# Optimization experiments

Hardware: AMD Instinct MI355X
Metric: run time of the kernel (lower is better)

## Reference

```python
import jax, jax.numpy as jnp
import numpy as np

T = 2048          # tokens (batch*seq flattened, vLLM style)
HID = 2048        # hidden size
NH = 16           # attention heads
QLR, KVLR = 1536, 512            # q / kv lora ranks
DN, DR, DV = 128, 64, 128        # qk_nope, qk_rope, v head dims
QKD = DN + DR                    # 192
INH, IHD = 16, 128               # indexer heads / head dim
ITOPK = 512                      # indexer top-k keys per query
E, EK, MI = 8, 4, 512            # routed experts, experts per token, expert intermediate
SH_MI = 1024                     # shared expert intermediate
EPS = 1e-6
ROUTED_SCALE = 1.0


def rms_norm(x, w, eps=EPS):
    v = jnp.mean(jnp.square(x), axis=-1, keepdims=True)
    return x * jax.lax.rsqrt(v + eps) * w


def layer_norm(x, w, b, eps=EPS):
    m = jnp.mean(x, axis=-1, keepdims=True)
    v = jnp.var(x, axis=-1, keepdims=True)
    return (x - m) * jax.lax.rsqrt(v + eps) * w + b


def rope(x, pos):
    """Neox-style rotary over the full last dim. x: [T, D] or [T, H, D]."""
    D = x.shape[-1]
    half = D // 2
    inv = 1.0 / (10000.0 ** (jnp.arange(half, dtype=jnp.float32) / half))
    f = pos.astype(jnp.float32)[:, None] * inv                  # [T, half]
    cos, sin = jnp.cos(f), jnp.sin(f)
    if x.ndim == 3:
        cos, sin = cos[:, None, :], sin[:, None, :]
    x1, x2 = x[..., :half], x[..., half:]
    return jnp.concatenate([x1 * cos - x2 * sin, x1 * sin + x2 * cos], axis=-1)


def setup_inputs() -> dict:
    key = jax.random.key(0)
    ks = jax.random.split(key, 16)

    def w(k, shape, fan_in):
        return (jax.random.normal(k, shape, jnp.float32) / np.sqrt(fan_in)).astype(jnp.float32)

    return {
        "positions": jnp.arange(T, dtype=jnp.int32),
        "hidden_states": jax.random.normal(ks[0], (T, HID), jnp.float32),
        "ln1_w": jnp.ones((HID,), jnp.float32),
        "ln2_w": jnp.ones((HID,), jnp.float32),
        "w_qkv_a": w(ks[1], (HID, QLR + KVLR + DR), HID),
        "q_a_ln_w": jnp.ones((QLR,), jnp.float32),
        "kv_a_ln_w": jnp.ones((KVLR,), jnp.float32),
        "w_q_b": w(ks[2], (QLR, NH * QKD), QLR),
        "w_kv_b": w(ks[3], (KVLR, NH * (DN + DV)), KVLR),
        "w_o": w(ks[4], (NH * DV, HID), NH * DV),
        "w_idx_k": w(ks[5], (HID, IHD), HID),
        "idx_k_ln_w": jnp.ones((IHD,), jnp.float32),
        "idx_k_ln_b": jnp.zeros((IHD,), jnp.float32),
        "w_idx_qb": w(ks[6], (QLR, INH * IHD), QLR),
        "w_idx_w": w(ks[7], (HID, INH), HID),
        "w_gate": w(ks[8], (HID, E), HID),
        "w_moe_gu": w(ks[9], (E, HID, 2 * MI), HID),
        "w_moe_d": w(ks[10], (E, MI, HID), MI),
        "w_sh_gu": w(ks[11], (HID, 2 * SH_MI), HID),
        "w_sh_d": w(ks[12], (SH_MI, HID), SH_MI),
    }


def reference(positions, hidden_states, ln1_w, ln2_w, w_qkv_a, q_a_ln_w, kv_a_ln_w,
              w_q_b, w_kv_b, w_o, w_idx_k, idx_k_ln_w, idx_k_ln_b, w_idx_qb,
              w_idx_w, w_gate, w_moe_gu, w_moe_d, w_sh_gu, w_sh_d):
    # residual is None on entry -> residual = hidden_states; h = rms_norm(h)
    residual = hidden_states
    h = rms_norm(hidden_states, ln1_w)

    # fused_qkv_a_proj -> split into q latent, kv latent, rope key
    qkv = h @ w_qkv_a
    q_c = rms_norm(qkv[:, :QLR], q_a_ln_w)                      # q_a_layernorm
    kv_c = rms_norm(qkv[:, QLR:QLR + KVLR], kv_a_ln_w)          # kv_a_layernorm
    k_pe = rope(qkv[:, QLR + KVLR:], positions)                 # [T, DR]

    # indexer key path: wk -> LayerNorm(w,b) -> rope on trailing DR dims
    idx_k = layer_norm(h @ w_idx_k, idx_k_ln_w, idx_k_ln_b)     # [T, IHD]
    idx_k = jnp.concatenate([idx_k[:, :IHD - DR], rope(idx_k[:, IHD - DR:], positions)], axis=-1)

    # query path: q_b projection, rope on the rope slice per head
    q = (q_c @ w_q_b).reshape(T, NH, QKD)
    q = jnp.concatenate([q[..., :DN], rope(q[..., DN:], positions)], axis=-1)

    # indexer query + per-query head weights (scale folds quant scale role in float ref)
    idx_q = (q_c @ w_idx_qb).reshape(T, INH, IHD)
    idx_q = jnp.concatenate([idx_q[..., :IHD - DR], rope(idx_q[..., IHD - DR:], positions)], axis=-1)
    idx_w = (h @ w_idx_w) * (IHD ** -0.5) * (INH ** -0.5)       # [T, INH]

    # lightning indexer: score[t,s] = sum_h w[t,h] * relu(q[t,h] . k[s])
    ilogits = jnp.einsum('thd,sd->ths', idx_q, idx_k)           # [T, INH, T]
    iscores = jnp.einsum('ths,th->ts', jax.nn.relu(ilogits), idx_w)
    causal = positions[:, None] >= positions[None, :]
    neg = jnp.finfo(iscores.dtype).min
    iscores = jnp.where(causal, iscores, neg)
    _, top_idx = jax.lax.top_k(iscores, ITOPK)                  # [T, ITOPK]
    sel = jnp.zeros((T, T), bool).at[jnp.arange(T)[:, None], top_idx].set(True)
    amask = sel & causal                                        # sparse attention mask

    # MLA attention (unabsorbed form): expand kv latent to per-head k_nope, v
    kv = (kv_c @ w_kv_b).reshape(T, NH, DN + DV)
    k_nope, v = kv[..., :DN], kv[..., DN:]
    alogits = (jnp.einsum('thd,shd->hts', q[..., :DN], k_nope)
               + jnp.einsum('thd,sd->hts', q[..., DN:], k_pe)) * (QKD ** -0.5)
    alogits = jnp.where(amask[None], alogits, neg)
    probs = jax.nn.softmax(alogits, axis=-1)
    attn = jnp.einsum('hts,shd->thd', probs, v).reshape(T, NH * DV)

    # o_proj + fused_add_rms_norm
    residual = residual + attn @ w_o
    h = rms_norm(residual, ln2_w)

    # MoE: softmax gate -> top-k, renormalize, dense combine + shared expert
    g = jax.nn.softmax(h @ w_gate, axis=-1)                     # [T, E]
    tv, ti = jax.lax.top_k(g, EK)
    tw = tv / jnp.sum(tv, axis=-1, keepdims=True)
    dense_w = jnp.zeros((T, E), h.dtype).at[jnp.arange(T)[:, None], ti].set(tw)
    gu = jnp.einsum('th,ehm->tem', h, w_moe_gu)                 # [T, E, 2*MI]
    act = jax.nn.silu(gu[..., :MI]) * gu[..., MI:]
    down = jnp.einsum('tem,emh->teh', act, w_moe_d)             # [T, E, HID]
    routed = jnp.einsum('teh,te->th', down, dense_w) * ROUTED_SCALE
    sgu = h @ w_sh_gu
    shared = (jax.nn.silu(sgu[:, :SH_MI]) * sgu[:, SH_MI:]) @ w_sh_d
    out = routed + shared
    return out, residual
```

## Files before the change

### kernel.cpp

```cpp
#include <hip/hip_runtime.h>
#include <cstdint>
#include <cstddef>

#define T_TOK 2048
#define HIDN  2048
#define NHEAD 16
#define QLRr  1536
#define KVLRr 512
#define DNn   128
#define DRr   64
#define DVv   128
#define QKDd  192
#define INHh  16
#define IHDd  128
#define ITOPKk 512
#define NEXP  8
#define MIi   512
#define SHMI  1024
#define EPSF  1e-6f
#define NEGINF (-3.402823466e38f)

typedef __attribute__((ext_vector_type(8))) short short8;
typedef __attribute__((ext_vector_type(4))) float float4v;

__device__ __forceinline__ float warp_sum(float v){
#pragma unroll
  for (int off=32; off>0; off>>=1) v += __shfl_down(v, off, 64);
  return v;
}
__device__ __forceinline__ float warp_max(float v){
#pragma unroll
  for (int off=32; off>0; off>>=1) v = fmaxf(v, __shfl_down(v, off, 64));
  return v;
}
__device__ __forceinline__ unsigned mapf(float f){
  unsigned b = __float_as_uint(f);
  if ((b<<1)==0u) b = 0u;
  return (b & 0x80000000u) ? ~b : (b | 0x80000000u);
}
__device__ __forceinline__ ushort f2bf(float f){
  unsigned u = __float_as_uint(f);
  unsigned r = (u + 0x7fffu + ((u>>16)&1u)) >> 16;
  return (ushort)r;
}
__device__ __forceinline__ float bf2f(ushort u){
  return __uint_as_float(((unsigned)u) << 16);
}

__global__ void rope_table_kernel(const int* __restrict__ pos,
                                  float* __restrict__ ct, float* __restrict__ st){
  int t = blockIdx.x, j = threadIdx.x;
  float inv = powf(10000.0f, -(float)j * (1.0f/32.0f));
  float f = (float)pos[t] * inv;
  ct[t*32+j] = cosf(f);
  st[t*32+j] = sinf(f);
}

__global__ __launch_bounds__(256) void rmsnorm_kernel(
    const float* __restrict__ x, int xstride, int xoff,
    const float* __restrict__ w, float* __restrict__ out, int ostride, int D){
  int t = blockIdx.x, tid = threadIdx.x;
  const float* xp = x + (size_t)t*xstride + xoff;
  const float4* x4 = (const float4*)xp;
  int D4 = D >> 2;
  float ss = 0.f;
  for (int i = tid; i < D4; i += 256){ float4 v = x4[i]; ss += v.x*v.x+v.y*v.y+v.z*v.z+v.w*v.w; }
  __shared__ float red[4];
  float s = warp_sum(ss);
  int lane = tid & 63, wid = tid >> 6;
  if (lane==0) red[wid] = s;
  __syncthreads();
  if (tid==0) red[0] = red[0]+red[1]+red[2]+red[3];
  __syncthreads();
  float sc = rsqrtf(red[0]/(float)D + EPSF);
  const float4* w4 = (const float4*)w;
  float4* o4 = (float4*)(out + (size_t)t*ostride);
  for (int i = tid; i < D4; i += 256){
    float4 v = x4[i], ww = w4[i];
    float4 r; r.x=v.x*sc*ww.x; r.y=v.y*sc*ww.y; r.z=v.z*sc*ww.z; r.w=v.w*sc*ww.w;
    o4[i] = r;
  }
}

__global__ void rope_kpe_kernel(const float* __restrict__ pe,
                                const float* __restrict__ ct, const float* __restrict__ st,
                                float* __restrict__ kpe){
  int t = blockIdx.x, j = threadIdx.x;
  const float* x = pe + (size_t)t*64;
  float x1 = x[j], x2 = x[32+j];
  float c = ct[t*32+j], sn = st[t*32+j];
  kpe[t*64+j]    = x1*c - x2*sn;
  kpe[t*64+32+j] = x1*sn + x2*c;
}

__global__ __launch_bounds__(128) void ln_rope_idxk_kernel(
    float* __restrict__ xk, const float* __restrict__ w, const float* __restrict__ b,
    const float* __restrict__ ct, const float* __restrict__ st){
  int t = blockIdx.x, tid = threadIdx.x;
  float v = xk[(size_t)t*IHDd + tid];
  float s1 = warp_sum(v), s2 = warp_sum(v*v);
  __shared__ float r1[2], r2[2];
  int lane = tid & 63, wid = tid >> 6;
  if (lane==0){ r1[wid]=s1; r2[wid]=s2; }
  __syncthreads();
  float mean = (r1[0]+r1[1]) * (1.f/128.f);
  float var  = (r2[0]+r2[1]) * (1.f/128.f) - mean*mean;
  float y = (v-mean)*rsqrtf(var+EPSF)*w[tid]+b[tid];
  __shared__ float ly[128];
  ly[tid] = y; __syncthreads();
  float o;
  if (tid < 64) o = y;
  else if (tid < 96){ int j = tid-64; o = ly[64+j]*ct[t*32+j] - ly[96+j]*st[t*32+j]; }
  else              { int j = tid-96; o = ly[64+j]*st[t*32+j] + ly[96+j]*ct[t*32+j]; }
  xk[(size_t)t*IHDd + tid] = o;
}

__global__ __launch_bounds__(256) void rope_q_kernel(float* __restrict__ q,
                                  const float* __restrict__ ct, const float* __restrict__ st){
  int t = blockIdx.x, tid = threadIdx.x;
  __shared__ float c[32], s[32];
  if (tid < 32){ c[tid]=ct[t*32+tid]; s[tid]=st[t*32+tid]; }
  __syncthreads();
  for (int idx = tid; idx < NHEAD*32; idx += 256){
    int hh = idx >> 5, j = idx & 31;
    float* base = q + (size_t)t*(NHEAD*QKDd) + hh*QKDd;
    float x1 = base[DNn+j], x2 = base[DNn+32+j];
    base[DNn+j]    = x1*c[j] - x2*s[j];
    base[DNn+32+j] = x1*s[j] + x2*c[j];
  }
}

__global__ __launch_bounds__(256) void rope_idxq_kernel(float* __restrict__ q,
                                  const float* __restrict__ ct, const float* __restrict__ st){
  int t = blockIdx.x, tid = threadIdx.x;
  __shared__ float c[32], s[32];
  if (tid < 32){ c[tid]=ct[t*32+tid]; s[tid]=st[t*32+tid]; }
  __syncthreads();
  for (int idx = tid; idx < INHh*32; idx += 256){
    int hh = idx >> 5, j = idx & 31;
    float* base = q + (size_t)t*(INHh*IHDd) + hh*IHDd;
    float x1 = base[64+j], x2 = base[96+j];
    base[64+j] = x1*c[j] - x2*s[j];
    base[96+j] = x1*s[j] + x2*c[j];
  }
}

__global__ __launch_bounds__(256) void gemm_f32(
    const float* __restrict__ A, int lda,
    const float* __restrict__ B, int ldb,
    float* __restrict__ C, int ldc,
    const float* __restrict__ addsrc, int ldadd,
    int M, int N, int K, float alpha){
  __shared__ float As[16][68];
  __shared__ float Bs[16][68];
  int tid = threadIdx.x;
  int tx = tid & 15, ty = tid >> 4;
  int m0 = blockIdx.y*64, n0 = blockIdx.x*64;
  float acc[4][4] = {};
  for (int k0 = 0; k0 < K; k0 += 16){
#pragma unroll
    for (int i = 0; i < 4; i++){
      int lin = tid + i*256; int r = lin >> 4, c = lin & 15;
      int m = m0 + r;
      As[c][r] = (m < M) ? A[(size_t)m*lda + k0 + c] : 0.f;
    }
#pragma unroll
    for (int i = 0; i < 4; i++){
      int lin = tid + i*256; int kk = lin >> 6, c = lin & 63;
      int n = n0 + c;
      Bs[kk][c] = (n < N) ? B[(size_t)(k0+kk)*ldb + n] : 0.f;
    }
    __syncthreads();
#pragma unroll
    for (int kk = 0; kk < 16; kk++){
      float4 av = *(const float4*)&As[kk][ty*4];
      float4 bv = *(const float4*)&Bs[kk][tx*4];
      float a[4] = {av.x, av.y, av.z, av.w};
      float b[4] = {bv.x, bv.y, bv.z, bv.w};
#pragma unroll
      for (int i = 0; i < 4; i++)
#pragma unroll
        for (int j = 0; j < 4; j++) acc[i][j] += a[i]*b[j];
    }
    __syncthreads();
  }
#pragma unroll
  for (int i = 0; i < 4; i++){
    int m = m0 + ty*4 + i;
    if (m >= M) continue;
#pragma unroll
    for (int j = 0; j < 4; j++){
      int n = n0 + tx*4 + j;
      if (n >= N) continue;
      float v = acc[i][j]*alpha;
      if (addsrc) v += addsrc[(size_t)m*ldadd + n];
      C[(size_t)m*ldc + n] = v;
    }
  }
}

__global__ __launch_bounds__(256) void conv_bf16(const float* __restrict__ in,
                                                 ushort* __restrict__ out, int n4){
  int i = blockIdx.x*256 + threadIdx.x;
  if (i < n4){
    float4 v = ((const float4*)in)[i];
    ushort4 o; o.x=f2bf(v.x); o.y=f2bf(v.y); o.z=f2bf(v.z); o.w=f2bf(v.w);
    ((ushort4*)out)[i] = o;
  }
}

__global__ __launch_bounds__(256) void split_bf16(const float* __restrict__ in,
                                                  ushort* __restrict__ hi,
                                                  ushort* __restrict__ lo, int n4){
  int i = blockIdx.x*256 + threadIdx.x;
  if (i >= n4) return;
  float4 v = ((const float4*)in)[i];
  ushort4 h, l;
  h.x = f2bf(v.x); l.x = f2bf(v.x - bf2f(h.x));
  h.y = f2bf(v.y); l.y = f2bf(v.y - bf2f(h.y));
  h.z = f2bf(v.z); l.z = f2bf(v.z - bf2f(h.z));
  h.w = f2bf(v.w); l.w = f2bf(v.w - bf2f(h.w));
  ((ushort4*)hi)[i] = h;
  ((ushort4*)lo)[i] = l;
}

__global__ __launch_bounds__(256) void transconv(const float* __restrict__ src0,
                                                 ushort* __restrict__ dst0, int K, int N){
  int e = blockIdx.z;
  const float* src = src0 + (size_t)e*K*N;
  ushort* dst = dst0 + (size_t)e*N*K;
  int k0 = blockIdx.y*32, n0 = blockIdx.x*32;
  __shared__ float tile[32][33];
  int c = threadIdx.x & 31, r = threadIdx.x >> 5;
  for (int rr = r; rr < 32; rr += 8) tile[rr][c] = src[(size_t)(k0+rr)*N + n0 + c];
  __syncthreads();
  for (int rr = r; rr < 32; rr += 8) dst[(size_t)(n0+rr)*K + k0 + c] = f2bf(tile[c][rr]);
}

__global__ __launch_bounds__(256) void transconv_split(const float* __restrict__ src,
                                                       ushort* __restrict__ dhi,
                                                       ushort* __restrict__ dlo, int K, int N){
  int k0 = blockIdx.y*32, n0 = blockIdx.x*32;
  __shared__ float tile[32][33];
  int c = threadIdx.x & 31, r = threadIdx.x >> 5;
  for (int rr = r; rr < 32; rr += 8) tile[rr][c] = src[(size_t)(k0+rr)*N + n0 + c];
  __syncthreads();
  for (int rr = r; rr < 32; rr += 8){
    float x = tile[c][rr];
    ushort h = f2bf(x);
    ushort l = f2bf(x - bf2f(h));
    size_t o = (size_t)(n0+rr)*K + k0 + c;
    dhi[o] = h; dlo[o] = l;
  }
}

__global__ __launch_bounds__(256) void gemm_b3(
    const ushort* __restrict__ Ah, const ushort* __restrict__ Al,
    const ushort* __restrict__ Bh, const ushort* __restrict__ Bl,
    float* __restrict__ C, const float* __restrict__ addsrc, int N, int K){
  __shared__ __align__(16) ushort Ahs[5120], Als[5120];
  __shared__ __align__(16) ushort Bhs[5120], Bls[5120];
  int tid = threadIdx.x, lane = tid & 63, w = tid >> 6;
  int m0 = blockIdx.y*128, n0 = blockIdx.x*128;
  int wr = w >> 1, wc = w & 1;
  int r15 = lane & 15, g = lane >> 4;
  int srow = tid >> 1, sh = (tid & 1) << 4;
  size_t arow = (size_t)(m0 + srow)*K + sh;
  size_t brow = (size_t)(n0 + srow)*K + sh;
  int soff = srow*40 + sh;
  int aoff[4], boff[4];
#pragma unroll
  for (int m = 0; m < 4; m++){
    aoff[m] = (wr*64 + m*16 + r15)*40 + g*8;
    boff[m] = (wc*64 + m*16 + r15)*40 + g*8;
  }
  float4v acc[4][4];
#pragma unroll
  for (int i=0;i<4;i++)
#pragma unroll
    for (int j=0;j<4;j++) acc[i][j] = (float4v){0.f,0.f,0.f,0.f};
  int nk = K >> 5;
  for (int kt = 0; kt < nk; kt++){
    int k0 = kt << 5;
    short8 ah0 = *(const short8*)(Ah + arow + k0);
    short8 ah1 = *(const short8*)(Ah + arow + k0 + 8);
    short8 al0 = *(const short8*)(Al + arow + k0);
    short8 al1 = *(const short8*)(Al + arow + k0 + 8);
    short8 bh0 = *(const short8*)(Bh + brow + k0);
    short8 bh1 = *(const short8*)(Bh + brow + k0 + 8);
    short8 bl0 = *(const short8*)(Bl + brow + k0);
    short8 bl1 = *(const short8*)(Bl + brow + k0 + 8);
    __syncthreads();
    *(short8*)&Ahs[soff] = ah0; *(short8*)&Ahs[soff+8] = ah1;
    *(short8*)&Als[soff] = al0; *(short8*)&Als[soff+8] = al1;
    *(short8*)&Bhs[soff] = bh0; *(short8*)&Bhs[soff+8] = bh1;
    *(short8*)&Bls[soff] = bl0; *(short8*)&Bls[soff+8] = bl1;
    __syncthreads();
    short8 avh[4], avl[4], bvh[4], bvl[4];
#pragma unroll
    for (int m = 0; m < 4; m++){
      avh[m] = *(const short8*)&Ahs[aoff[m]];
      avl[m] = *(const short8*)&Als[aoff[m]];
    }
#pragma unroll
    for (int n = 0; n < 4; n++){
      bvh[n] = *(const short8*)&Bhs[boff[n]];
      bvl[n] = *(const short8*)&Bls[boff[n]];
    }
#pragma unroll
    for (int m = 0; m < 4; m++)
#pragma unroll
      for (int n = 0; n < 4; n++){
        acc[m][n] = __builtin_amdgcn_mfma_f32_16x16x32_bf16(avh[m], bvh[n], acc[m][n], 0, 0, 0);
        acc[m][n] = __builtin_amdgcn_mfma_f32_16x16x32_bf16(avl[m], bvh[n], acc[m][n], 0, 0, 0);
        acc[m][n] = __builtin_amdgcn_mfma_f32_16x16x32_bf16(avh[m], bvl[n], acc[m][n], 0, 0, 0);
      }
  }
#pragma unroll
  for (int m = 0; m < 4; m++){
    int row0 = m0 + wr*64 + m*16 + g*4;
#pragma unroll
    for (int n = 0; n < 4; n++){
      int col = n0 + wc*64 + n*16 + r15;
#pragma unroll
      for (int r = 0; r < 4; r++){
        float v = acc[m][n][r];
        size_t o = (size_t)(row0 + r)*N + col;
        if (addsrc) v += addsrc[o];
        C[o] = v;
      }
    }
  }
}

template<int OUTBF>
__global__ __launch_bounds__(256) void gemm_bf16s(
    const ushort* __restrict__ A, const ushort* __restrict__ Bt,
    float* __restrict__ Cf, ushort* __restrict__ Cb,
    const float* __restrict__ addsrc, int N, int K){
  __shared__ __align__(16) ushort As[5120];
  __shared__ __align__(16) ushort Bs[5120];
  int tid = threadIdx.x, lane = tid & 63, w = tid >> 6;
  int m0 = blockIdx.y*128, n0 = blockIdx.x*128;
  int wr = w >> 1, wc = w & 1;
  int r15 = lane & 15, g = lane >> 4;
  int srow = tid >> 1, sh = (tid & 1) << 4;
  const ushort* Ag = A + (size_t)(m0 + srow)*K + sh;
  const ushort* Bg = Bt + (size_t)(n0 + srow)*K + sh;
  ushort* Asw = &As[srow*40 + sh];
  ushort* Bsw = &Bs[srow*40 + sh];
  int aoff[4], boff[4];
#pragma unroll
  for (int m = 0; m < 4; m++){
    aoff[m] = (wr*64 + m*16 + r15)*40 + g*8;
    boff[m] = (wc*64 + m*16 + r15)*40 + g*8;
  }
  float4v acc[4][4];
#pragma unroll
  for (int i=0;i<4;i++)
#pragma unroll
    for (int j=0;j<4;j++) acc[i][j] = (float4v){0.f,0.f,0.f,0.f};
  int nk = K >> 5;
  for (int kt = 0; kt < nk; kt++){
    int k0 = kt << 5;
    short8 a0 = *(const short8*)(Ag + k0);
    short8 a1 = *(const short8*)(Ag + k0 + 8);
    short8 b0 = *(const short8*)(Bg + k0);
    short8 b1 = *(const short8*)(Bg + k0 + 8);
    __syncthreads();
    *(short8*)Asw = a0; *(short8*)(Asw + 8) = a1;
    *(short8*)Bsw = b0; *(short8*)(Bsw + 8) = b1;
    __syncthreads();
    short8 av[4], bv[4];
#pragma unroll
    for (int m = 0; m < 4; m++) av[m] = *(const short8*)&As[aoff[m]];
#pragma unroll
    for (int n = 0; n < 4; n++) bv[n] = *(const short8*)&Bs[boff[n]];
#pragma unroll
    for (int m = 0; m < 4; m++)
#pragma unroll
      for (int n = 0; n < 4; n++)
        acc[m][n] = __builtin_amdgcn_mfma_f32_16x16x32_bf16(av[m], bv[n], acc[m][n], 0, 0, 0);
  }
#pragma unroll
  for (int m = 0; m < 4; m++){
    int row0 = m0 + wr*64 + m*16 + g*4;
#pragma unroll
    for (int n = 0; n < 4; n++){
      int col = n0 + wc*64 + n*16 + r15;
#pragma unroll
      for (int r = 0; r < 4; r++){
        float v = acc[m][n][r];
        size_t o = (size_t)(row0 + r)*N + col;
        if (addsrc) v += addsrc[o];
        if (OUTBF) Cb[o] = f2bf(v);
        else       Cf[o] = v;
      }
    }
  }
}

__global__ __launch_bounds__(256) void moe_gemm1s(
    const ushort* __restrict__ h2bf, const ushort* __restrict__ wgut,
    const int* __restrict__ ecnt, const int* __restrict__ elist,
    float* __restrict__ gu){
  int e = blockIdx.z;
  int count = ecnt[e];
  int r0 = blockIdx.y*128;
  if (r0 >= count) return;
  __shared__ int rows[128];
  __shared__ __align__(16) ushort As[5120];
  __shared__ __align__(16) ushort Bs[5120];
  int tid = threadIdx.x, lane = tid & 63, w = tid >> 6;
  int n0 = blockIdx.x*128;
  if (tid < 128) rows[tid] = (r0 + tid < count) ? elist[e*2048 + r0 + tid] : -1;
  __syncthreads();
  int wr = w >> 1, wc = w & 1;
  int r15 = lane & 15, g = lane >> 4;
  int srow = tid >> 1, sh = (tid & 1) << 4;
  int ent0 = rows[srow];
  int tok = (ent0 >= 0) ? (ent0 >> 2) : 0;
  const ushort* Ag = h2bf + (size_t)tok*2048 + sh;
  const ushort* Bg = wgut + ((size_t)e*1024 + n0 + srow)*2048 + sh;
  ushort* Asw = &As[srow*40 + sh];
  ushort* Bsw = &Bs[srow*40 + sh];
  int aoff[4], boff[4];
#pragma unroll
  for (int m = 0; m < 4; m++){
    aoff[m] = (wr*64 + m*16 + r15)*40 + g*8;
    boff[m] = (wc*64 + m*16 + r15)*40 + g*8;
  }
  float4v acc[4][4];
#pragma unroll
  for (int i=0;i<4;i++)
#pragma unroll
    for (int j=0;j<4;j++) acc[i][j] = (float4v){0.f,0.f,0.f,0.f};
  for (int kt = 0; kt < 64; kt++){
    int k0 = kt << 5;
    short8 a0 = *(const short8*)(Ag + k0);
    short8 a1 = *(const short8*)(Ag + k0 + 8);
    short8 b0 = *(const short8*)(Bg + k0);
    short8 b1 = *(const short8*)(Bg + k0 + 8);
    __syncthreads();
    *(short8*)Asw = a0; *(short8*)(Asw + 8) = a1;
    *(short8*)Bsw = b0; *(short8*)(Bsw + 8) = b1;
    __syncthreads();
    short8 av[4], bv[4];
#pragma unroll
    for (int m = 0; m < 4; m++) av[m] = *(const short8*)&As[aoff[m]];
#pragma unroll
    for (int n = 0; n < 4; n++) bv[n] = *(const short8*)&Bs[boff[n]];
#pragma unroll
    for (int m = 0; m < 4; m++)
#pragma unroll
      for (int n = 0; n < 4; n++)
        acc[m][n] = __builtin_amdgcn_mfma_f32_16x16x32_bf16(av[m], bv[n], acc[m][n], 0, 0, 0);
  }
#pragma unroll
  for (int m = 0; m < 4; m++){
#pragma unroll
    for (int r = 0; r < 4; r++){
      int ent = rows[wr*64 + m*16 + g*4 + r];
      if (ent < 0) continue;
#pragma unroll
      for (int n = 0; n < 4; n++){
        int col = n0 + wc*64 + n*16 + r15;
        gu[(size_t)ent*1024 + col] = acc[m][n][r];
      }
    }
  }
}

__global__ __launch_bounds__(256) void moe_gemm2s(
    const ushort* __restrict__ act, const ushort* __restrict__ wdt,
    const int* __restrict__ ecnt, const int* __restrict__ elist,
    const float* __restrict__ tw, float* __restrict__ down){
  int e = blockIdx.z;
  int count = ecnt[e];
  int r0 = blockIdx.y*128;
  if (r0 >= count) return;
  __shared__ int rows[128];
  __shared__ __align__(16) ushort As[5120];
  __shared__ __align__(16) ushort Bs[5120];
  int tid = threadIdx.x, lane = tid & 63, w = tid >> 6;
  int n0 = blockIdx.x*128;
  if (tid < 128) rows[tid] = (r0 + tid < count) ? elist[e*2048 + r0 + tid] : -1;
  __syncthreads();
  int wr = w >> 1, wc = w & 1;
  int r15 = lane & 15, g = lane >> 4;
  int srow = tid >> 1, sh = (tid & 1) << 4;
  int ent0 = rows[srow];
  int src = (ent0 >= 0) ? ent0 : 0;
  const ushort* Ag = act + (size_t)src*512 + sh;
  const ushort* Bg = wdt + ((size_t)e*2048 + n0 + srow)*512 + sh;
  ushort* Asw = &As[srow*40 + sh];
  ushort* Bsw = &Bs[srow*40 + sh];
  int aoff[4], boff[4];
#pragma unroll
  for (int m = 0; m < 4; m++){
    aoff[m] = (wr*64 + m*16 + r15)*40 + g*8;
    boff[m] = (wc*64 + m*16 + r15)*40 + g*8;
  }
  float4v acc[4][4];
#pragma unroll
  for (int i=0;i<4;i++)
#pragma unroll
    for (int j=0;j<4;j++) acc[i][j] = (float4v){0.f,0.f,0.f,0.f};
  for (int kt = 0; kt < 16; kt++){
    int k0 = kt << 5;
    short8 a0 = *(const short8*)(Ag + k0);
    short8 a1 = *(const short8*)(Ag + k0 + 8);
    short8 b0 = *(const short8*)(Bg + k0);
    short8 b1 = *(const short8*)(Bg + k0 + 8);
    __syncthreads();
    *(short8*)Asw = a0; *(short8*)(Asw + 8) = a1;
    *(short8*)Bsw = b0; *(short8*)(Bsw + 8) = b1;
    __syncthreads();
    short8 av[4], bv[4];
#pragma unroll
    for (int m = 0; m < 4; m++) av[m] = *(const short8*)&As[aoff[m]];
#pragma unroll
    for (int n = 0; n < 4; n++) bv[n] = *(const short8*)&Bs[boff[n]];
#pragma unroll
    for (int m = 0; m < 4; m++)
#pragma unroll
      for (int n = 0; n < 4; n++)
        acc[m][n] = __builtin_amdgcn_mfma_f32_16x16x32_bf16(av[m], bv[n], acc[m][n], 0, 0, 0);
  }
#pragma unroll
  for (int m = 0; m < 4; m++){
#pragma unroll
    for (int r = 0; r < 4; r++){
      int ent = rows[wr*64 + m*16 + g*4 + r];
      if (ent < 0) continue;
      float wgt = tw[ent];
#pragma unroll
      for (int n = 0; n < 4; n++){
        int col = n0 + wc*64 + n*16 + r15;
        down[(size_t)ent*2048 + col] = acc[m][n][r]*wgt;
      }
    }
  }
}

__global__ __launch_bounds__(256) void iscores_kernel(
    const float* __restrict__ idx_q, const float* __restrict__ idx_k,
    const float* __restrict__ idx_w, float* __restrict__ sc){
  int sb = blockIdx.x, tb = blockIdx.y;
  if (sb > tb) return;
  int t0 = tb*64, s0 = sb*64;
  __shared__ float As[32][68];
  __shared__ float Bs[32][68];
  __shared__ float Ws[64][17];
  int tid = threadIdx.x, tx = tid & 15, ty = tid >> 4;
  for (int i = tid; i < 1024; i += 256){ int r = i >> 4, hh = i & 15; Ws[r][hh] = idx_w[(size_t)(t0+r)*16 + hh]; }
  float sco[4][4] = {};
  for (int h = 0; h < 16; h++){
    float acc[4][4] = {};
    for (int k0 = 0; k0 < 128; k0 += 32){
#pragma unroll
      for (int i = 0; i < 8; i++){
        int lin = tid + i*256; int r = lin >> 5, c = lin & 31;
        As[c][r] = idx_q[(size_t)(t0+r)*2048 + h*128 + k0 + c];
      }
#pragma unroll
      for (int i = 0; i < 8; i++){
        int lin = tid + i*256; int r = lin >> 5, c = lin & 31;
        Bs[c][r] = idx_k[(size_t)(s0+r)*128 + k0 + c];
      }
      __syncthreads();
#pragma unroll
      for (int kk = 0; kk < 32; kk++){
        float4 av = *(const float4*)&As[kk][ty*4];
        float4 bv = *(const float4*)&Bs[kk][tx*4];
        float a[4] = {av.x, av.y, av.z, av.w};
        float b[4] = {bv.x, bv.y, bv.z, bv.w};
#pragma unroll
        for (int i = 0; i < 4; i++)
#pragma unroll
          for (int j = 0; j < 4; j++) acc[i][j] += a[i]*b[j];
      }
      __syncthreads();
    }
#pragma unroll
    for (int i = 0; i < 4; i++){
      float wv = Ws[ty*4+i][h];
#pragma unroll
      for (int j = 0; j < 4; j++) sco[i][j] += wv * fmaxf(acc[i][j], 0.f);
    }
  }
#pragma unroll
  for (int i = 0; i < 4; i++){
    int tg = t0 + ty*4 + i;
#pragma unroll
    for (int j = 0; j < 4; j++){
      int sg = s0 + tx*4 + j;
      sc[(size_t)tg*2048 + sg] = (sg <= tg) ? sco[i][j] : NEGINF;
    }
  }
}

__global__ __launch_bounds__(256) void topk_kernel(
    const float* __restrict__ scores, int* __restrict__ list, int* __restrict__ cnt){
  int t = blockIdx.x, tid = threadIdx.x;
  if (t < ITOPKk){
    for (int i = tid; i <= t; i += 256) list[(size_t)t*ITOPKk + i] = i;
    if (tid==0) cnt[t] = t+1;
    return;
  }
  int n = t+1;
  const float* row = scores + (size_t)t*2048;
  __shared__ unsigned hist[256];
  __shared__ unsigned sh_prefix, sh_krem;
  __shared__ int scan[256];
  __shared__ int sh_base_sel, sh_base_eq;
  if (tid==0){ sh_prefix = 0u; sh_krem = ITOPKk; }
  __syncthreads();
  for (int level = 3; level >= 0; level--){
    int shift = level*8;
    hist[tid] = 0u; __syncthreads();
    unsigned pfx = sh_prefix;
    for (int s = tid; s < n; s += 256){
      unsigned u = mapf(row[s]);
      bool ok = (level==3) || ((u >> (shift+8)) == pfx);
      if (ok) atomicAdd(&hist[(u >> shift) & 255u], 1u);
    }
    __syncthreads();
    if (tid==0){
      unsigned krem = sh_krem, c = 0u; int bsel = 0;
      for (int b = 255; b >= 0; b--){
        if (c + hist[b] >= krem){ bsel = b; break; }
        c += hist[b];
      }
      sh_prefix = (pfx << 8) | (unsigned)bsel;
      sh_krem = krem - c;
    }
    __syncthreads();
  }
  unsigned uth = sh_prefix; int R = (int)sh_krem;
  if (tid==0){ sh_base_sel = 0; sh_base_eq = 0; }
  __syncthreads();
  for (int c0 = 0; c0 < n; c0 += 256){
    int s = c0 + tid;
    unsigned u = (s < n) ? mapf(row[s]) : 0u;
    int gt = (s < n) && (u > uth);
    int eq = (s < n) && (u == uth);
    scan[tid] = (eq << 16) | gt; __syncthreads();
    for (int off = 1; off < 256; off <<= 1){
      int v = (tid >= off) ? scan[tid-off] : 0; __syncthreads();
      scan[tid] += v; __syncthreads();
    }
    int incl = scan[tid];
    int gt_incl = incl & 0xffff, eq_incl = incl >> 16;
    int gt_excl = gt_incl - gt, eq_excl = eq_incl - eq;
    int tot = scan[255]; int gt_tot = tot & 0xffff, eq_tot = tot >> 16;
    int base_sel = sh_base_sel, base_eq = sh_base_eq;
    int rtake = R - base_eq; if (rtake < 0) rtake = 0;
    bool selected = gt || (eq && eq_excl < rtake);
    int pos = base_sel + gt_excl + min(eq_excl, rtake);
    if (selected) list[(size_t)t*ITOPKk + pos] = s;
    __syncthreads();
    if (tid==0){
      sh_base_sel = base_sel + gt_tot + min(eq_tot, rtake);
      sh_base_eq  = base_eq + eq_tot;
    }
    __syncthreads();
  }
  if (tid==0) cnt[t] = ITOPKk;
}

#define HG 2
__global__ __launch_bounds__(256) void attn_kernel(
    const float* __restrict__ q, const float* __restrict__ kv,
    const float* __restrict__ kpe,
    const int* __restrict__ list, const int* __restrict__ cnt,
    float* __restrict__ attn){
  int b = blockIdx.x;
  int g8 = b & 7, t = b >> 3;
  int h0 = g8*HG;
  int tid = threadIdx.x, lane = tid & 63, w = tid >> 6;
  __shared__ int   sl[ITOPKk];
  __shared__ float qs[HG][200];
  __shared__ float lg[HG][ITOPKk];
  __shared__ float redm[4], reds[4];
  __shared__ float4 outp4[8][32];
  int n = cnt[t];
  for (int i = tid; i < n; i += 256) sl[i] = list[(size_t)t*ITOPKk + i];
  for (int i = tid; i < HG*192; i += 256){
    int hh = i/192, d = i - hh*192;
    qs[hh][d] = q[(size_t)t*(NHEAD*QKDd) + (h0+hh)*QKDd + d];
  }
  __syncthreads();
  const float scale = 0.07216878364870323f;
  int half = lane >> 5, l5 = lane & 31;
  for (int i = w; i < n; i += 4){
    int s = sl[i];
    float4 k4 = *(const float4*)(kv + (size_t)s*4096 + (h0+half)*256 + l5*4);
    float2 pe2 = *(const float2*)(kpe + (size_t)s*64 + l5*2);
    float4 qv = *(const float4*)&qs[half][l5*4];
    float pk = k4.x*qv.x + k4.y*qv.y + k4.z*qv.z + k4.w*qv.w;
    pk += pe2.x*qs[half][128 + l5*2] + pe2.y*qs[half][128 + l5*2 + 1];
    pk += __shfl_down(pk, 16, 32);
    pk += __shfl_down(pk, 8, 32);
    pk += __shfl_down(pk, 4, 32);
    pk += __shfl_down(pk, 2, 32);
    pk += __shfl_down(pk, 1, 32);
    if (l5 == 0) lg[half][i] = pk*scale;
  }
  __syncthreads();
  int slice = tid & 31, sg = tid >> 5;
  for (int hh = 0; hh < HG; hh++){
    int h = h0 + hh;
    float mx = NEGINF;
    for (int i = tid; i < n; i += 256) mx = fmaxf(mx, lg[hh][i]);
    mx = warp_max(mx);
    if (lane==0) redm[w] = mx;
    __syncthreads();
    mx = fmaxf(fmaxf(redm[0],redm[1]), fmaxf(redm[2],redm[3]));
    float sum = 0.f;
    for (int i = tid; i < n; i += 256){ float p = expf(lg[hh][i]-mx); lg[hh][i] = p; sum += p; }
    sum = warp_sum(sum);
    if (lane==0) reds[w] = sum;
    __syncthreads();
    float inv = 1.f/(reds[0]+reds[1]+reds[2]+reds[3]);
    float4 acc = {0,0,0,0};
    for (int i = sg; i < n; i += 8){
      float p = lg[hh][i];
      float4 v4 = *((const float4*)(kv + (size_t)sl[i]*4096 + h*256 + 128) + slice);
      acc.x += p*v4.x; acc.y += p*v4.y; acc.z += p*v4.z; acc.w += p*v4.w;
    }
    outp4[sg][slice] = acc;
    __syncthreads();
    if (tid < 32){
      float4 r = outp4[0][tid];
#pragma unroll
      for (int gg = 1; gg < 8; gg++){
        float4 o = outp4[gg][tid];
        r.x += o.x; r.y += o.y; r.z += o.z; r.w += o.w;
      }
      r.x *= inv; r.y *= inv; r.z *= inv; r.w *= inv;
      *(float4*)&attn[(size_t)t*2048 + h*128 + tid*4] = r;
    }
    __syncthreads();
  }
}

__global__ void gate_kernel(const float* __restrict__ glog, float* __restrict__ tw,
                            int* __restrict__ ecnt, int* __restrict__ elist){
  int t = blockIdx.x*256 + threadIdx.x;
  if (t >= T_TOK) return;
  float g[8]; float mx = NEGINF;
  for (int i = 0; i < 8; i++){ g[i] = glog[t*8+i]; mx = fmaxf(mx, g[i]); }
  float s = 0.f;
  for (int i = 0; i < 8; i++){ g[i] = expf(g[i]-mx); s += g[i]; }
  for (int i = 0; i < 8; i++) g[i] /= s;
  bool used[8] = {};
  float tv[4]; int si[4];
  for (int k = 0; k < 4; k++){
    float best = -1.f; int bi = 0;
    for (int i = 0; i < 8; i++) if (!used[i] && g[i] > best){ best = g[i]; bi = i; }
    used[bi] = true; tv[k] = best; si[k] = bi;
  }
  float s4 = tv[0]+tv[1]+tv[2]+tv[3];
  for (int k = 0; k < 4; k++){
    tw[t*4+k] = tv[k]/s4;
    int pos = atomicAdd(&ecnt[si[k]], 1);
    elist[si[k]*2048 + pos] = t*4+k;
  }
}

__global__ __launch_bounds__(256) void silu_moe(const float* __restrict__ gu,
                                                ushort* __restrict__ act){
  int i = blockIdx.x*256 + threadIdx.x;
  if (i >= 8192*128) return;
  int row = i >> 7, jc = i & 127;
  float4 g4 = ((const float4*)(gu + (size_t)row*1024))[jc];
  float4 u4 = ((const float4*)(gu + (size_t)row*1024 + 512))[jc];
  ushort4 o;
  o.x = f2bf(g4.x/(1.f+expf(-g4.x))*u4.x);
  o.y = f2bf(g4.y/(1.f+expf(-g4.y))*u4.y);
  o.z = f2bf(g4.z/(1.f+expf(-g4.z))*u4.z);
  o.w = f2bf(g4.w/(1.f+expf(-g4.w))*u4.w);
  ((ushort4*)(act + (size_t)row*512))[jc] = o;
}

__global__ __launch_bounds__(256) void moe_combine(const float* __restrict__ down,
                                                   float* __restrict__ outf){
  int t = blockIdx.x;
  size_t base = (size_t)t*4*2048;
  for (int d = threadIdx.x; d < 2048; d += 256){
    float s = down[base+d] + down[base+2048+d] + down[base+4096+d] + down[base+6144+d];
    outf[(size_t)t*2048 + d] += s;
  }
}

__global__ __launch_bounds__(256) void silu_sh(const float* __restrict__ sgu,
                                               ushort* __restrict__ shact){
  int i = blockIdx.x*256 + threadIdx.x;
  if (i >= 2048*256) return;
  int row = i >> 8, jc = i & 255;
  float4 g4 = ((const float4*)(sgu + (size_t)row*2048))[jc];
  float4 u4 = ((const float4*)(sgu + (size_t)row*2048 + 1024))[jc];
  ushort4 o;
  o.x = f2bf(g4.x/(1.f+expf(-g4.x))*u4.x);
  o.y = f2bf(g4.y/(1.f+expf(-g4.y))*u4.y);
  o.z = f2bf(g4.z/(1.f+expf(-g4.z))*u4.z);
  o.w = f2bf(g4.w/(1.f+expf(-g4.w))*u4.w);
  ((ushort4*)(shact + (size_t)row*1024))[jc] = o;
}

extern "C" void kernel_launch(void* const* d_in, const int* in_sizes, int n_in,
                              void* d_out, int out_size, void* d_ws, size_t ws_size,
                              hipStream_t stream){
  const int*   positions  = (const int*)  d_in[0];
  const float* hidden     = (const float*)d_in[1];
  const float* ln1_w      = (const float*)d_in[2];
  const float* ln2_w      = (const float*)d_in[3];
  const float* w_qkv_a    = (const float*)d_in[4];
  const float* q_a_ln_w   = (const float*)d_in[5];
  const float* kv_a_ln_w  = (const float*)d_in[6];
  const float* w_q_b      = (const float*)d_in[7];
  const float* w_kv_b     = (const float*)d_in[8];
  const float* w_o        = (const float*)d_in[9];
  const float* w_idx_k    = (const float*)d_in[10];
  const float* idx_k_ln_w = (const float*)d_in[11];
  const float* idx_k_ln_b = (const float*)d_in[12];
  const float* w_idx_qb   = (const float*)d_in[13];
  const float* w_idx_w    = (const float*)d_in[14];
  const float* w_gate     = (const float*)d_in[15];
  const float* w_moe_gu   = (const float*)d_in[16];
  const float* w_moe_d    = (const float*)d_in[17];
  const float* w_sh_gu    = (const float*)d_in[18];
  const float* w_sh_d     = (const float*)d_in[19];

  float* out_final = (float*)d_out;
  float* residual  = (float*)d_out + (size_t)T_TOK*HIDN;

  float* ws = (float*)d_ws;
  float* arena   = ws;
  float* qkv_main= arena;
  float* qkv_pe  = arena + 4194304;
  float* iscores = arena;
  float* qbuf    = arena + 4325376;
  float* idx_q   = arena + 10616832;
  float* q_c     = arena + 14811136;
  float* kv_c    = arena + 17956864;
  float* sgu     = arena;
  float* gu_buf  = arena;
  float* down_buf= arena;
  ushort* act_bf = (ushort*)(arena + 16777216);
  ushort* h_hi  = (ushort*)(arena + 4325376);
  ushort* h_lo  = h_hi + 4194304;
  ushort* wqa_hi= (ushort*)(arena + 8519680);
  ushort* wqa_lo= wqa_hi + 4325376;
  ushort* wik_hi= (ushort*)(arena + 12845056);
  ushort* wik_lo= wik_hi + 262144;
  ushort* qc2_hi= (ushort*)arena;
  ushort* qc2_lo= qc2_hi + 3145728;
  ushort* wiq_hi= (ushort*)(arena + 4325376);
  ushort* wiq_lo= wiq_hi + 3145728;
  ushort* s1 = (ushort*)arena;
  ushort* s2 = (ushort*)(arena + 10616832);
  size_t off = 19005440;
  float* h      = ws + off; off += 4194304;
  float* kv     = ws + off; off += 8388608;
  float* attnbuf= ws + off; off += 4194304;
  float* k_pe   = ws + off; off += 131072;
  float* idx_k  = ws + off; off += 262144;
  float* idx_w  = ws + off; off += 32768;
  float* glog   = ws + off; off += 16384;
  float* tw     = ws + off; off += 8192;
  float* ctab   = ws + off; off += 65536;
  float* stab   = ws + off; off += 65536;
  int* list     = (int*)(ws + off);
  int* cnt      = list + 1048576;
  int* ecnt     = cnt + 2048;
  int* elist    = ecnt + 8;
  off += 1067016;
  ushort* h2_bf   = (ushort*)(ws + off);
  off += 2097152;
  ushort* shact_bf= (ushort*)(ws + off);
  off += 1048576;
  ushort* wshgu_t = (ushort*)(ws + off);
  off += 2097152;
  ushort* wshd_t  = (ushort*)(ws + off);
  off += 1048576;
  ushort* wmgu_t = (ushort*)kv;
  ushort* wmd_t  = (ushort*)attnbuf;
  size_t total_bytes = off * sizeof(float);
  if (ws_size < total_bytes) return;

  ushort* qc_hi  = s1;
  ushort* qc_lo  = s1 + 3145728;
  ushort* wqbt_hi= s2;
  ushort* wqbt_lo= s2 + 4718592;
  ushort* kvc_hi = s1;
  ushort* kvc_lo = s1 + 1048576;
  ushort* wkvt_hi= s1 + 2097152;
  ushort* wkvt_lo= s1 + 4194304;
  ushort* at_hi  = s2;
  ushort* at_lo  = s2 + 4194304;
  ushort* wot_hi = s1;
  ushort* wot_lo = s1 + 4194304;

  transconv<<<dim3(64,64,1), 256, 0, stream>>>(w_sh_gu, wshgu_t, 2048, 2048);
  transconv<<<dim3(64,32,1), 256, 0, stream>>>(w_sh_d,  wshd_t,  1024, 2048);

  rope_table_kernel<<<T_TOK, 32, 0, stream>>>(positions, ctab, stab);
  rmsnorm_kernel<<<T_TOK, 256, 0, stream>>>(hidden, HIDN, 0, ln1_w, h, HIDN, HIDN);
  split_bf16<<<4096, 256, 0, stream>>>(h, h_hi, h_lo, 1048576);
  transconv_split<<<dim3(66,64), 256, 0, stream>>>(w_qkv_a, wqa_hi, wqa_lo, 2048, 2112);
  gemm_b3<<<dim3(16,16), 256, 0, stream>>>(h_hi, h_lo, wqa_hi, wqa_lo, qkv_main, nullptr, 2048, 2048);
  gemm_f32<<<dim3(1,32), 256, 0, stream>>>(h, HIDN, w_qkv_a + 2048, 2112, qkv_pe, 64, nullptr, 0, T_TOK, 64, HIDN, 1.f);
  rmsnorm_kernel<<<T_TOK, 256, 0, stream>>>(qkv_main, 2048, 0,    q_a_ln_w,  q_c,  QLRr,  QLRr);
  rmsnorm_kernel<<<T_TOK, 256, 0, stream>>>(qkv_main, 2048, QLRr, kv_a_ln_w, kv_c, KVLRr, KVLRr);
  rope_kpe_kernel<<<T_TOK, 32, 0, stream>>>(qkv_pe, ctab, stab, k_pe);
  transconv_split<<<dim3(4,64), 256, 0, stream>>>(w_idx_k, wik_hi, wik_lo, 2048, 128);
  gemm_b3<<<dim3(1,16), 256, 0, stream>>>(h_hi, h_lo, wik_hi, wik_lo, idx_k, nullptr, 128, 2048);
  ln_rope_idxk_kernel<<<T_TOK, 128, 0, stream>>>(idx_k, idx_k_ln_w, idx_k_ln_b, ctab, stab);
  split_bf16<<<3072, 256, 0, stream>>>(q_c, qc2_hi, qc2_lo, 786432);
  transconv_split<<<dim3(64,48), 256, 0, stream>>>(w_idx_qb, wiq_hi, wiq_lo, 1536, 2048);
  gemm_b3<<<dim3(16,16), 256, 0, stream>>>(qc2_hi, qc2_lo, wiq_hi, wiq_lo, idx_q, nullptr, 2048, 1536);
  rope_idxq_kernel<<<T_TOK, 256, 0, stream>>>(idx_q, ctab, stab);
  gemm_f32<<<dim3(1,32), 256, 0, stream>>>(h, HIDN, w_idx_w, INHh, idx_w, INHh, nullptr, 0, T_TOK, INHh, HIDN, 0.02209708691207961f);
  iscores_kernel<<<dim3(32,32), 256, 0, stream>>>(idx_q, idx_k, idx_w, iscores);
  topk_kernel<<<T_TOK, 256, 0, stream>>>(iscores, list, cnt);
  split_bf16<<<3072, 256, 0, stream>>>(q_c, qc_hi, qc_lo, 786432);
  transconv_split<<<dim3(96,48), 256, 0, stream>>>(w_q_b, wqbt_hi, wqbt_lo, 1536, 3072);
  gemm_b3<<<dim3(24,16), 256, 0, stream>>>(qc_hi, qc_lo, wqbt_hi, wqbt_lo, qbuf, nullptr, 3072, 1536);
  rope_q_kernel<<<T_TOK, 256, 0, stream>>>(qbuf, ctab, stab);
  split_bf16<<<1024, 256, 0, stream>>>(kv_c, kvc_hi, kvc_lo, 262144);
  transconv_split<<<dim3(128,16), 256, 0, stream>>>(w_kv_b, wkvt_hi, wkvt_lo, 512, 4096);
  gemm_b3<<<dim3(32,16), 256, 0, stream>>>(kvc_hi, kvc_lo, wkvt_hi, wkvt_lo, kv, nullptr, 4096, 512);
  attn_kernel<<<T_TOK*(NHEAD/HG), 256, 0, stream>>>(qbuf, kv, k_pe, list, cnt, attnbuf);
  split_bf16<<<4096, 256, 0, stream>>>(attnbuf, at_hi, at_lo, 1048576);
  transconv_split<<<dim3(64,64), 256, 0, stream>>>(w_o, wot_hi, wot_lo, 2048, 2048);
  gemm_b3<<<dim3(16,16), 256, 0, stream>>>(at_hi, at_lo, wot_hi, wot_lo, residual, hidden, 2048, 2048);
  transconv<<<dim3(32,64,8), 256, 0, stream>>>(w_moe_gu, wmgu_t, 2048, 1024);
  transconv<<<dim3(64,16,8), 256, 0, stream>>>(w_moe_d,  wmd_t,  512,  2048);
  rmsnorm_kernel<<<T_TOK, 256, 0, stream>>>(residual, HIDN, 0, ln2_w, h, HIDN, HIDN);
  gemm_f32<<<dim3(1,32), 256, 0, stream>>>(h, HIDN, w_gate, NEXP, glog, NEXP, nullptr, 0, T_TOK, NEXP, HIDN, 1.f);
  hipMemsetAsync(ecnt, 0, NEXP*sizeof(int), stream);
  gate_kernel<<<8, 256, 0, stream>>>(glog, tw, ecnt, elist);
  conv_bf16<<<4096, 256, 0, stream>>>(h, h2_bf, 1048576);
  gemm_bf16s<0><<<dim3(16,16), 256, 0, stream>>>(h2_bf, wshgu_t, sgu, nullptr, nullptr, 2048, 2048);
  silu_sh<<<2048, 256, 0, stream>>>(sgu, shact_bf);
  gemm_bf16s<0><<<dim3(16,16), 256, 0, stream>>>(shact_bf, wshd_t, out_final, nullptr, nullptr, 2048, 1024);
  moe_gemm1s<<<dim3(8, 16, NEXP), 256, 0, stream>>>(h2_bf, wmgu_t, ecnt, elist, gu_buf);
  silu_moe<<<4096, 256, 0, stream>>>(gu_buf, act_bf);
  moe_gemm2s<<<dim3(16, 16, NEXP), 256, 0, stream>>>(act_bf, wmd_t, ecnt, elist, tw, down_buf);
  moe_combine<<<T_TOK, 256, 0, stream>>>(down_buf, out_final);
  (void)in_sizes; (void)n_in; (void)out_size;
}
```

Measured before the change: 2.760 ms.

## Compute indexer scores with split-bf16 MFMA and reuse the q_c bf16 split

Replaces the fp32 SIMT indexer-score kernel with a 128x128-tile MFMA kernel. It uses a three-product hi/lo bf16 split to keep near-fp32 accuracy, and applies the per-head ReLU and weighted sum in the accumulator epilogue. Adds split_bf16 passes for idx_q and idx_k. The q_c split is now done once and shared by the indexer and q_b GEMMs. Workspace aliases are reshuffled (qc and kvc moved into the kv and attnbuf regions, kv_c split moved earlier) so the new buffers don't clobber live data. The explicit causal -inf fill on diagonal tiles is dropped, which relies on topk reading only the first t+1 entries.

```diff
diff --git a/kernel.cpp b/kernel.cpp
--- a/kernel.cpp
+++ b/kernel.cpp
@@ -333,6 +333,107 @@
   }
 }
 
+__global__ __launch_bounds__(256) void iscores_b3(
+    const ushort* __restrict__ iqh, const ushort* __restrict__ iql,
+    const ushort* __restrict__ ikh, const ushort* __restrict__ ikl,
+    const float* __restrict__ idx_w,
+    float* __restrict__ sc){
+  int sb = blockIdx.x, tb = blockIdx.y;
+  if (sb > tb) return;
+  int t0 = tb*128, s0 = sb*128;
+  __shared__ __align__(16) ushort Ahs[5120], Als[5120];
+  __shared__ __align__(16) ushort Bhs[5120], Bls[5120];
+  __shared__ float wlds[128][17];
+  int tid = threadIdx.x, lane = tid & 63, w = tid >> 6;
+  int wr = w >> 1, wc = w & 1;
+  int r15 = lane & 15, g = lane >> 4;
+  int srow = tid >> 1, sh = (tid & 1) << 4;
+  for (int i = tid; i < 2048; i += 256){
+    int r = i >> 4, hh = i & 15;
+    wlds[r][hh] = idx_w[(size_t)(t0+r)*16 + hh];
+  }
+  int soff = srow*40 + sh;
+  int aoff[4], boff[4];
+#pragma unroll
+  for (int m = 0; m < 4; m++){
+    aoff[m] = (wr*64 + m*16 + r15)*40 + g*8;
+    boff[m] = (wc*64 + m*16 + r15)*40 + g*8;
+  }
+  float4v sco[4][4];
+#pragma unroll
+  for (int i=0;i<4;i++)
+#pragma unroll
+    for (int j=0;j<4;j++) sco[i][j] = (float4v){0.f,0.f,0.f,0.f};
+  for (int h = 0; h < 16; h++){
+    float4v acc[4][4];
+#pragma unroll
+    for (int i=0;i<4;i++)
+#pragma unroll
+      for (int j=0;j<4;j++) acc[i][j] = (float4v){0.f,0.f,0.f,0.f};
+    size_t arow = ((size_t)(t0 + srow)*16 + h)*128 + sh;
+    size_t brow = (size_t)(s0 + srow)*128 + sh;
+#pragma unroll
+    for (int kt = 0; kt < 4; kt++){
+      int k0 = kt << 5;
+      short8 ah0 = *(const short8*)(iqh + arow + k0);
+      short8 ah1 = *(const short8*)(iqh + arow + k0 + 8);
+      short8 al0 = *(const short8*)(iql + arow + k0);
+      short8 al1 = *(const short8*)(iql + arow + k0 + 8);
+      short8 bh0 = *(const short8*)(ikh + brow + k0);
+      short8 bh1 = *(const short8*)(ikh + brow + k0 + 8);
+      short8 bl0 = *(const short8*)(ikl + brow + k0);
+      short8 bl1 = *(const short8*)(ikl + brow + k0 + 8);
+      __syncthreads();
+      *(short8*)&Ahs[soff] = ah0; *(short8*)&Ahs[soff+8] = ah1;
+      *(short8*)&Als[soff] = al0; *(short8*)&Als[soff+8] = al1;
+      *(short8*)&Bhs[soff] = bh0; *(short8*)&Bhs[soff+8] = bh1;
+      *(short8*)&Bls[soff] = bl0; *(short8*)&Bls[soff+8] = bl1;
+      __syncthreads();
+      short8 avh[4], avl[4], bvh[4], bvl[4];
+#pragma unroll
+      for (int m = 0; m < 4; m++){
+        avh[m] = *(const short8*)&Ahs[aoff[m]];
+        avl[m] = *(const short8*)&Als[aoff[m]];
+      }
+#pragma unroll
+      for (int n = 0; n < 4; n++){
+        bvh[n] = *(const short8*)&Bhs[boff[n]];
+        bvl[n] = *(const short8*)&Bls[boff[n]];
+      }
+#pragma unroll
+      for (int m = 0; m < 4; m++)
+#pragma unroll
+        for (int n = 0; n < 4; n++){
+          acc[m][n] = __builtin_amdgcn_mfma_f32_16x16x32_bf16(avh[m], bvh[n], acc[m][n], 0, 0, 0);
+          acc[m][n] = __builtin_amdgcn_mfma_f32_16x16x32_bf16(avl[m], bvh[n], acc[m][n], 0, 0, 0);
+          acc[m][n] = __builtin_amdgcn_mfma_f32_16x16x32_bf16(avh[m], bvl[n], acc[m][n], 0, 0, 0);
+        }
+    }
+#pragma unroll
+    for (int m = 0; m < 4; m++){
+      int rbase = wr*64 + m*16 + g*4;
+#pragma unroll
+      for (int r = 0; r < 4; r++){
+        float wv = wlds[rbase + r][h];
+#pragma unroll
+        for (int n = 0; n < 4; n++)
+          sco[m][n][r] += wv * fmaxf(acc[m][n][r], 0.f);
+      }
+    }
+  }
+#pragma unroll
+  for (int m = 0; m < 4; m++){
+    int row0 = t0 + wr*64 + m*16 + g*4;
+#pragma unroll
+    for (int n = 0; n < 4; n++){
+      int col = s0 + wc*64 + n*16 + r15;
+#pragma unroll
+      for (int r = 0; r < 4; r++)
+        sc[(size_t)(row0 + r)*2048 + col] = sco[m][n][r];
+    }
+  }
+}
+
 template<int OUTBF>
 __global__ __launch_bounds__(256) void gemm_bf16s(
     const ushort* __restrict__ A, const ushort* __restrict__ Bt,
@@ -539,63 +640,6 @@
         int col = n0 + wc*64 + n*16 + r15;
         down[(size_t)ent*2048 + col] = acc[m][n][r]*wgt;
       }
-    }
-  }
-}
-
-__global__ __launch_bounds__(256) void iscores_kernel(
-    const float* __restrict__ idx_q, const float* __restrict__ idx_k,
-    const float* __restrict__ idx_w, float* __restrict__ sc){
-  int sb = blockIdx.x, tb = blockIdx.y;
-  if (sb > tb) return;
-  int t0 = tb*64, s0 = sb*64;
-  __shared__ float As[32][68];
-  __shared__ float Bs[32][68];
-  __shared__ float Ws[64][17];
-  int tid = threadIdx.x, tx = tid & 15, ty = tid >> 4;
-  for (int i = tid; i < 1024; i += 256){ int r = i >> 4, hh = i & 15; Ws[r][hh] = idx_w[(size_t)(t0+r)*16 + hh]; }
-  float sco[4][4] = {};
-  for (int h = 0; h < 16; h++){
-    float acc[4][4] = {};
-    for (int k0 = 0; k0 < 128; k0 += 32){
-#pragma unroll
-      for (int i = 0; i < 8; i++){
-        int lin = tid + i*256; int r = lin >> 5, c = lin & 31;
-        As[c][r] = idx_q[(size_t)(t0+r)*2048 + h*128 + k0 + c];
-      }
-#pragma unroll
-      for (int i = 0; i < 8; i++){
-        int lin = tid + i*256; int r = lin >> 5, c = lin & 31;
-        Bs[c][r] = idx_k[(size_t)(s0+r)*128 + k0 + c];
-      }
-      __syncthreads();
-#pragma unroll
-      for (int kk = 0; kk < 32; kk++){
-        float4 av = *(const float4*)&As[kk][ty*4];
-        float4 bv = *(const float4*)&Bs[kk][tx*4];
-        float a[4] = {av.x, av.y, av.z, av.w};
-        float b[4] = {bv.x, bv.y, bv.z, bv.w};
-#pragma unroll
-        for (int i = 0; i < 4; i++)
-#pragma unroll
-          for (int j = 0; j < 4; j++) acc[i][j] += a[i]*b[j];
-      }
-      __syncthreads();
-    }
-#pragma unroll
-    for (int i = 0; i < 4; i++){
-      float wv = Ws[ty*4+i][h];
-#pragma unroll
-      for (int j = 0; j < 4; j++) sco[i][j] += wv * fmaxf(acc[i][j], 0.f);
-    }
-  }
-#pragma unroll
-  for (int i = 0; i < 4; i++){
-    int tg = t0 + ty*4 + i;
-#pragma unroll
-    for (int j = 0; j < 4; j++){
-      int sg = s0 + tx*4 + j;
-      sc[(size_t)tg*2048 + sg] = (sg <= tg) ? sco[i][j] : NEGINF;
     }
   }
 }
@@ -855,10 +899,12 @@
   ushort* wqa_lo= wqa_hi + 4325376;
   ushort* wik_hi= (ushort*)(arena + 12845056);
   ushort* wik_lo= wik_hi + 262144;
-  ushort* qc2_hi= (ushort*)arena;
-  ushort* qc2_lo= qc2_hi + 3145728;
   ushort* wiq_hi= (ushort*)(arena + 4325376);
   ushort* wiq_lo= wiq_hi + 3145728;
+  ushort* ik_hi = (ushort*)(arena + 4325376);
+  ushort* ik_lo = ik_hi + 262144;
+  ushort* iq_hi = (ushort*)(arena + 14811136);
+  ushort* iq_lo = iq_hi + 4194304;
   ushort* s1 = (ushort*)arena;
   ushort* s2 = (ushort*)(arena + 10616832);
   size_t off = 19005440;
@@ -877,27 +923,23 @@
   int* ecnt     = cnt + 2048;
   int* elist    = ecnt + 8;
   off += 1067016;
-  ushort* h2_bf   = (ushort*)(ws + off);
-  off += 2097152;
-  ushort* shact_bf= (ushort*)(ws + off);
-  off += 1048576;
-  ushort* wshgu_t = (ushort*)(ws + off);
-  off += 2097152;
-  ushort* wshd_t  = (ushort*)(ws + off);
-  off += 1048576;
+  ushort* h2_bf   = (ushort*)(ws + off); off += 2097152;
+  ushort* shact_bf= (ushort*)(ws + off); off += 1048576;
+  ushort* wshgu_t = (ushort*)(ws + off); off += 2097152;
+  ushort* wshd_t  = (ushort*)(ws + off); off += 1048576;
+  ushort* qc_hi  = (ushort*)kv;
+  ushort* qc_lo  = qc_hi + 3145728;
+  ushort* kvc_hi = (ushort*)attnbuf;
+  ushort* kvc_lo = kvc_hi + 1048576;
   ushort* wmgu_t = (ushort*)kv;
   ushort* wmd_t  = (ushort*)attnbuf;
   size_t total_bytes = off * sizeof(float);
   if (ws_size < total_bytes) return;
 
-  ushort* qc_hi  = s1;
-  ushort* qc_lo  = s1 + 3145728;
   ushort* wqbt_hi= s2;
   ushort* wqbt_lo= s2 + 4718592;
-  ushort* kvc_hi = s1;
-  ushort* kvc_lo = s1 + 1048576;
-  ushort* wkvt_hi= s1 + 2097152;
-  ushort* wkvt_lo= s1 + 4194304;
+  ushort* wkvt_hi= s1;
+  ushort* wkvt_lo= s1 + 2097152;
   ushort* at_hi  = s2;
   ushort* at_lo  = s2 + 4194304;
   ushort* wot_hi = s1;
@@ -918,18 +960,19 @@
   transconv_split<<<dim3(4,64), 256, 0, stream>>>(w_idx_k, wik_hi, wik_lo, 2048, 128);
   gemm_b3<<<dim3(1,16), 256, 0, stream>>>(h_hi, h_lo, wik_hi, wik_lo, idx_k, nullptr, 128, 2048);
   ln_rope_idxk_kernel<<<T_TOK, 128, 0, stream>>>(idx_k, idx_k_ln_w, idx_k_ln_b, ctab, stab);
-  split_bf16<<<3072, 256, 0, stream>>>(q_c, qc2_hi, qc2_lo, 786432);
+  split_bf16<<<3072, 256, 0, stream>>>(q_c, qc_hi, qc_lo, 786432);
   transconv_split<<<dim3(64,48), 256, 0, stream>>>(w_idx_qb, wiq_hi, wiq_lo, 1536, 2048);
-  gemm_b3<<<dim3(16,16), 256, 0, stream>>>(qc2_hi, qc2_lo, wiq_hi, wiq_lo, idx_q, nullptr, 2048, 1536);
+  gemm_b3<<<dim3(16,16), 256, 0, stream>>>(qc_hi, qc_lo, wiq_hi, wiq_lo, idx_q, nullptr, 2048, 1536);
   rope_idxq_kernel<<<T_TOK, 256, 0, stream>>>(idx_q, ctab, stab);
+  split_bf16<<<1024, 256, 0, stream>>>(idx_k, ik_hi, ik_lo, 65536);
+  split_bf16<<<1024, 256, 0, stream>>>(kv_c, kvc_hi, kvc_lo, 262144);
+  split_bf16<<<4096, 256, 0, stream>>>(idx_q, iq_hi, iq_lo, 1048576);
   gemm_f32<<<dim3(1,32), 256, 0, stream>>>(h, HIDN, w_idx_w, INHh, idx_w, INHh, nullptr, 0, T_TOK, INHh, HIDN, 0.02209708691207961f);
-  iscores_kernel<<<dim3(32,32), 256, 0, stream>>>(idx_q, idx_k, idx_w, iscores);
+  iscores_b3<<<dim3(16,16), 256, 0, stream>>>(iq_hi, iq_lo, ik_hi, ik_lo, idx_w, iscores);
   topk_kernel<<<T_TOK, 256, 0, stream>>>(iscores, list, cnt);
-  split_bf16<<<3072, 256, 0, stream>>>(q_c, qc_hi, qc_lo, 786432);
   transconv_split<<<dim3(96,48), 256, 0, stream>>>(w_q_b, wqbt_hi, wqbt_lo, 1536, 3072);
   gemm_b3<<<dim3(24,16), 256, 0, stream>>>(qc_hi, qc_lo, wqbt_hi, wqbt_lo, qbuf, nullptr, 3072, 1536);
   rope_q_kernel<<<T_TOK, 256, 0, stream>>>(qbuf, ctab, stab);
-  split_bf16<<<1024, 256, 0, stream>>>(kv_c, kvc_hi, kvc_lo, 262144);
   transconv_split<<<dim3(128,16), 256, 0, stream>>>(w_kv_b, wkvt_hi, wkvt_lo, 512, 4096);
   gemm_b3<<<dim3(32,16), 256, 0, stream>>>(kvc_hi, kvc_lo, wkvt_hi, wkvt_lo, kv, nullptr, 4096, 512);
   attn_kernel<<<T_TOK*(NHEAD/HG), 256, 0, stream>>>(qbuf, kv, k_pe, list, cnt, attnbuf);
```

Result: faster. 2.540 ms (-8.0%).
